# Kernel tuning notes

Measured on AMD Instinct MI355X. Metric: run time of the kernel, lower is better.

## Reference

```python
import jax, jax.numpy as jnp
import numpy as np

N_NODES = 50000
N_EDGES = 800000
F_NODE = 128
F_TASK = 128
HID = 64
HEADS = 4
BATCH = 16
NEG_SLOPE = 0.2


def setup_inputs() -> dict:
    key = jax.random.key(0)
    ks = jax.random.split(key, 20)
    rn = lambda k, sh, s=0.05: jax.random.normal(k, sh, dtype=jnp.float32) * s
    return {
        "x": rn(ks[0], (N_NODES, F_NODE), 1.0),
        "edge_index": jax.random.randint(ks[1], (2, N_EDGES), 0, N_NODES, dtype=jnp.int32),
        "task_feat": rn(ks[2], (BATCH, F_TASK), 1.0),
        # GAT layer 1 (F_NODE -> HEADS*HID, concat)
        "W1": rn(ks[3], (F_NODE, HEADS * HID)),
        "att_src1": rn(ks[4], (HEADS, HID)),
        "att_dst1": rn(ks[5], (HEADS, HID)),
        "b1": jnp.zeros((HEADS * HID,), jnp.float32),
        # GAT layer 2 (HEADS*HID -> HID, 1 head, mean/no-concat)
        "W2": rn(ks[6], (HEADS * HID, HID)),
        "att_src2": rn(ks[7], (1, HID)),
        "att_dst2": rn(ks[8], (1, HID)),
        "b2": jnp.zeros((HID,), jnp.float32),
        # task encoder MLP
        "te_W1": rn(ks[9], (F_TASK, HID)),
        "te_b1": jnp.zeros((HID,), jnp.float32),
        "te_W2": rn(ks[10], (HID, HID)),
        "te_b2": jnp.zeros((HID,), jnp.float32),
        # classifier MLP (2*HID -> HID -> 1)
        "cl_W1": rn(ks[11], (2 * HID, HID)),
        "cl_b1": jnp.zeros((HID,), jnp.float32),
        "cl_W2": rn(ks[12], (HID, 1)),
        "cl_b2": jnp.zeros((1,), jnp.float32),
    }


def _gat(x, src, dst, W, a_src, a_dst, bias, concat):
    """PyG-style GATConv: self-loops, per-dst segment softmax, scatter-add."""
    n = x.shape[0]
    heads, ch = a_src.shape
    h = (x @ W).reshape(n, heads, ch)                       # [N,H,C]
    alpha_s = jnp.einsum("nhc,hc->nh", h, a_src)            # [N,H]
    alpha_d = jnp.einsum("nhc,hc->nh", h, a_dst)
    loop = jnp.arange(n, dtype=src.dtype)                   # add self-loops
    s = jnp.concatenate([src, loop])
    d = jnp.concatenate([dst, loop])
    e = jax.nn.leaky_relu(alpha_s[s] + alpha_d[d], NEG_SLOPE)   # [E+N,H]
    m = jax.lax.stop_gradient(jax.ops.segment_max(e, d, num_segments=n))
    ex = jnp.exp(e - m[d])
    den = jax.ops.segment_sum(ex, d, num_segments=n)
    alpha = ex / (den[d] + 1e-16)                           # [E+N,H]
    out = jax.ops.segment_sum(h[s] * alpha[:, :, None], d, num_segments=n)
    out = out.reshape(n, heads * ch) if concat else out.mean(axis=1)
    return out + bias


def reference(x, edge_index, task_feat, W1, att_src1, att_dst1, b1,
              W2, att_src2, att_dst2, b2, te_W1, te_b1, te_W2, te_b2,
              cl_W1, cl_b1, cl_W2, cl_b2):
    src, dst = edge_index[0], edge_index[1]
    h = jax.nn.elu(_gat(x, src, dst, W1, att_src1, att_dst1, b1, True))
    h = jax.nn.elu(_gat(h, src, dst, W2, att_src2, att_dst2, b2, False))  # [N,HID]
    t = jax.nn.relu(task_feat @ te_W1 + te_b1) @ te_W2 + te_b2            # [B,HID]
    # classifier on concat([h_exp, t_exp]) == split first linear into two halves
    Wh, Wt = cl_W1[:HID], cl_W1[HID:]
    z = jax.nn.relu((h @ Wh)[None, :, :] + (t @ Wt)[:, None, :] + cl_b1)  # [B,N,HID]
    scores = (z @ cl_W2)[..., 0] + cl_b2[0]                               # [B,N]
    return scores
```

## Files before the change

### kernel.cpp

```cpp
#include <hip/hip_runtime.h>
#include <hip/hip_fp16.h>

#define NN 50000
#define NE 800000
#define FN 128
#define HH 256
#define HID 64
#define NBKT 196
#define CHUNK 4000
#define REGCAP 8192

typedef _Float16 f16x8 __attribute__((ext_vector_type(8)));
typedef float f32x4 __attribute__((ext_vector_type(4)));

__device__ __forceinline__ float lrelu(float v){ return v >= 0.f ? v : 0.2f * v; }
__device__ __forceinline__ float elu_(float v){ return v > 0.f ? v : expm1f(v); }

__device__ __forceinline__ void unp4(const float2 r, float& f0, float& f1, float& f2, float& f3){
  const __half2* hp = (const __half2*)&r;
  float2 a = __half22float2(hp[0]);
  float2 b = __half22float2(hp[1]);
  f0 = a.x; f1 = a.y; f2 = b.x; f3 = b.y;
}

__global__ void k_misc(const float* __restrict__ W2, const float* __restrict__ W1,
                       __half* __restrict__ Bp, __half* __restrict__ Bp1, __half* __restrict__ Bwh,
                       const float* __restrict__ task, const float* __restrict__ W1t,
                       const float* __restrict__ b1t, const float* __restrict__ W2t,
                       const float* __restrict__ b2t, const float* __restrict__ clW1,
                       const float* __restrict__ clb1, float* __restrict__ tWb,
                       int* __restrict__ binCnt){
  int bid = blockIdx.x, t = threadIdx.x;
  if (bid < 26){
    int f = bid * 256 + t;
    if (f < 2048){
      int lane = f & 63;
      int ct = (f >> 6) & 3, kt = f >> 8;
      int kbase = kt * 32 + (lane >> 4) * 8;
      int col = ct * 16 + (lane & 15);
#pragma unroll
      for (int i = 0; i < 8; ++i)
        Bp[(size_t)f * 8 + i] = (__half)W2[(kbase + i) * HID + col];
    } else if (f < 6144){
      int g = f - 2048;
      int lane = g & 63;
      int ct = (g >> 6) & 15, kt = g >> 10;
      int kbase = kt * 32 + (lane >> 4) * 8;
      int col = ct * 16 + (lane & 15);
#pragma unroll
      for (int i = 0; i < 8; ++i)
        Bp1[(size_t)g * 8 + i] = (__half)W1[(kbase + i) * HH + col];
    } else {
      int g = f - 6144;
      int lane = g & 63;
      int ct = (g >> 6) & 3, kt = g >> 8;
      int kbase = kt * 32 + (lane >> 4) * 8;
      int col = ct * 16 + (lane & 15);
#pragma unroll
      for (int i = 0; i < 8; ++i)
        Bwh[(size_t)g * 8 + i] = (__half)clW1[(kbase + i) * HID + col];
    }
  } else {
    binCnt[t] = 0;
    __shared__ float t1[16][64];
    __shared__ float t2[16][64];
    for (int idx = t; idx < 1024; idx += 256){
      int b = idx >> 6, c = idx & 63;
      float acc = b1t[c];
      for (int k = 0; k < 128; ++k) acc = fmaf(task[b*128 + k], W1t[k*64 + c], acc);
      t1[b][c] = fmaxf(acc, 0.f);
    }
    __syncthreads();
    for (int idx = t; idx < 1024; idx += 256){
      int b = idx >> 6, c = idx & 63;
      float acc = b2t[c];
      for (int k = 0; k < 64; ++k) acc = fmaf(t1[b][k], W2t[k*64 + c], acc);
      t2[b][c] = acc;
    }
    __syncthreads();
    for (int idx = t; idx < 1024; idx += 256){
      int b = idx >> 6, c = idx & 63;
      float acc = clb1[c];
      for (int k = 0; k < 64; ++k) acc = fmaf(t2[b][k], clW1[(64 + k)*64 + c], acc);
      tWb[idx] = acc;
    }
  }
}

__global__ void k_binGemm(const int* __restrict__ ei, int* __restrict__ binCnt,
                          unsigned* __restrict__ pr,
                          const float* __restrict__ x, const __half* __restrict__ Bp1,
                          const float* __restrict__ as1, const float* __restrict__ ad1,
                          __half* __restrict__ h1h, float* __restrict__ als, float* __restrict__ ald){
  __shared__ int hist[NBKT];
  __shared__ int lstart[NBKT];
  __shared__ int gpos[NBKT];
  __shared__ int cnt[NBKT];
  __shared__ unsigned stage[CHUNK];
  int bid = blockIdx.x, t = threadIdx.x;
  if (bid < 200){
    int e_base = bid * CHUNK;
    if (t < NBKT){ hist[t] = 0; cnt[t] = 0; }
    __syncthreads();
    for (int i = t; i < CHUNK; i += 256)
      atomicAdd(&hist[ei[NE + e_base + i] >> 8], 1);
    __syncthreads();
    {
      int lane = t & 63, wvi = t >> 6;
      int v = (t < NBKT) ? hist[t] : 0;
      int iv = v;
#pragma unroll
      for (int off = 1; off < 64; off <<= 1){
        int u = __shfl_up(iv, off);
        if (lane >= off) iv += u;
      }
      __shared__ int wsum[4];
      if (lane == 63) wsum[wvi] = iv;
      __syncthreads();
      int add = 0;
      for (int w = 0; w < wvi; ++w) add += wsum[w];
      iv += add;
      if (t < NBKT){
        lstart[t] = iv - v;
        gpos[t] = (v > 0) ? atomicAdd(&binCnt[t], v) : 0;
      }
    }
    __syncthreads();
    for (int i = t; i < CHUNK; i += 256){
      int e = e_base + i;
      int s = ei[e], d = ei[NE + e];
      int bb = d >> 8;
      int r = atomicAdd(&cnt[bb], 1);
      stage[lstart[bb] + r] = (unsigned)s | ((unsigned)(d & 255) << 16) | ((unsigned)bb << 24);
    }
    __syncthreads();
    for (int i = t; i < CHUNK; i += 256){
      unsigned p = stage[i];
      int bb = p >> 24;
      pr[(size_t)bb * REGCAP + gpos[bb] + (i - lstart[bb])] = p;
    }
    return;
  }
  int blk = bid - 200;
  int wv = t >> 6, lane = t & 63;
  int n0 = blk * 64 + wv * 16;
  int arow = n0 + (lane & 15);
  if (arow > NN - 1) arow = NN - 1;
  const float* xbase = x + (size_t)arow * FN + (lane >> 4) * 8;
  const f16x8* bbase = (const f16x8*)Bp1 + lane;

  f32x4 acc[16];
#pragma unroll
  for (int ct = 0; ct < 16; ++ct) acc[ct] = (f32x4){0.f,0.f,0.f,0.f};

#pragma unroll
  for (int kt = 0; kt < 4; ++kt){
    float4 xa = *(const float4*)(xbase + kt * 32);
    float4 xb = *(const float4*)(xbase + kt * 32 + 4);
    f16x8 a;
    a[0] = (_Float16)xa.x; a[1] = (_Float16)xa.y; a[2] = (_Float16)xa.z; a[3] = (_Float16)xa.w;
    a[4] = (_Float16)xb.x; a[5] = (_Float16)xb.y; a[6] = (_Float16)xb.z; a[7] = (_Float16)xb.w;
#pragma unroll
    for (int ct = 0; ct < 16; ++ct)
      acc[ct] = __builtin_amdgcn_mfma_f32_16x16x32_f16(a, bbase[(kt*16 + ct) * 64], acc[ct], 0, 0, 0);
  }

  int c4 = lane & 15, g4 = lane >> 4;
#pragma unroll
  for (int ct = 0; ct < 16; ++ct){
#pragma unroll
    for (int i = 0; i < 4; ++i){
      int n = n0 + g4 * 4 + i;
      if (n < NN) h1h[(size_t)n * HH + ct * 16 + c4] = (__half)acc[ct][i];
    }
  }
#pragma unroll
  for (int h = 0; h < 4; ++h){
    float sa0 = as1[(h*4+0)*16 + c4], sa1 = as1[(h*4+1)*16 + c4];
    float sa2 = as1[(h*4+2)*16 + c4], sa3 = as1[(h*4+3)*16 + c4];
    float da0 = ad1[(h*4+0)*16 + c4], da1 = ad1[(h*4+1)*16 + c4];
    float da2 = ad1[(h*4+2)*16 + c4], da3 = ad1[(h*4+3)*16 + c4];
#pragma unroll
    for (int i = 0; i < 4; ++i){
      float vs = acc[h*4+0][i]*sa0 + acc[h*4+1][i]*sa1 + acc[h*4+2][i]*sa2 + acc[h*4+3][i]*sa3;
      float vd = acc[h*4+0][i]*da0 + acc[h*4+1][i]*da1 + acc[h*4+2][i]*da2 + acc[h*4+3][i]*da3;
#pragma unroll
      for (int off = 1; off < 16; off <<= 1){
        vs += __shfl_xor(vs, off);
        vd += __shfl_xor(vd, off);
      }
      if (c4 == 0){
        int n = n0 + g4 * 4 + i;
        if (n < NN){ als[n*4 + h] = vs; ald[n*4 + h] = vd; }
      }
    }
  }
}

__global__ void k_rsplace(const int* __restrict__ binCnt, const unsigned* __restrict__ pr,
                          int* __restrict__ rs, int* __restrict__ csr){
  __shared__ int bbase[256];
  __shared__ int hist[256];
  __shared__ int lp[256];
  __shared__ int wsA[4];
  __shared__ int wsB[4];
  int b = blockIdx.x, t = threadIdx.x;
  int lane = t & 63, wv = t >> 6;
  {
    int v = (t < NBKT) ? binCnt[t] : 0;
    int iv = v;
#pragma unroll
    for (int off = 1; off < 64; off <<= 1){
      int u = __shfl_up(iv, off);
      if (lane >= off) iv += u;
    }
    if (lane == 63) wsA[wv] = iv;
    __syncthreads();
    int add = 0;
    for (int w = 0; w < wv; ++w) add += wsA[w];
    bbase[t] = iv + add - v;
    hist[t] = 0;
  }
  __syncthreads();
  int myBase = bbase[b];
  int myCnt  = binCnt[b];
  const unsigned* reg = pr + (size_t)b * REGCAP;
  for (int i = t; i < myCnt; i += 256)
    atomicAdd(&hist[(reg[i] >> 16) & 255], 1);
  __syncthreads();
  int excl;
  {
    int v = hist[t];
    int iv = v;
#pragma unroll
    for (int off = 1; off < 64; off <<= 1){
      int u = __shfl_up(iv, off);
      if (lane >= off) iv += u;
    }
    if (lane == 63) wsB[wv] = iv;
    __syncthreads();
    int add = 0;
    for (int w = 0; w < wv; ++w) add += wsB[w];
    excl = myBase + iv + add - v;
    lp[t] = excl;
  }
  int idx = b * 256 + t;
  if (idx < NN) rs[idx] = excl;
  if (b == 0 && t == 0) rs[NN] = NE;
  __syncthreads();
  for (int i = t; i < myCnt; i += 256){
    unsigned p = reg[i];
    int pos = atomicAdd(&lp[(p >> 16) & 255], 1);
    csr[pos] = (int)(p & 0xFFFFu);
  }
}

__global__ void k_agg1m(const int* __restrict__ rs, const int* __restrict__ csr,
                        const __half* __restrict__ h1h, const float* __restrict__ als,
                        const float* __restrict__ ald, const float* __restrict__ b1,
                        __half* __restrict__ g1h){
  int t = threadIdx.x, wv = t >> 6, lane = t & 63;
  int head = lane >> 4, q = lane & 15;
  int n = blockIdx.x * 4 + wv;
  int e0 = rs[n], e1 = rs[n + 1];
  int deg = e1 - e0;
  float adh = ald[n*4 + head];

  float w0r = 0.f, w1r = 0.f, w2r = 0.f, w3r = 0.f;
  int   s0r = 0,   s1r = 0,   s2r = 0,   s3r = 0;
  float den = 0.f;
  if (q      < deg){ s0r = csr[e0 + q];      w0r = expf(lrelu(als[s0r*4+head] + adh)); den += w0r; }
  if (q + 16 < deg){ s1r = csr[e0 + 16 + q]; w1r = expf(lrelu(als[s1r*4+head] + adh)); den += w1r; }
  if (q + 32 < deg){ s2r = csr[e0 + 32 + q]; w2r = expf(lrelu(als[s2r*4+head] + adh)); den += w2r; }
  if (q + 48 < deg){ s3r = csr[e0 + 48 + q]; w3r = expf(lrelu(als[s3r*4+head] + adh)); den += w3r; }
  for (int e = e0 + 64 + q; e < e1; e += 16) den += expf(lrelu(als[csr[e]*4+head] + adh));
  den += __shfl_xor(den, 1); den += __shfl_xor(den, 2);
  den += __shfl_xor(den, 4); den += __shfl_xor(den, 8);
  float selfw = expf(lrelu(als[n*4+head] + adh));
  float inv = 1.f / (den + selfw + 1e-16f);
  float wself = selfw * inv;

  float a0, a1, a2, a3;
  { float2 r = *(const float2*)(h1h + (size_t)n * HH + lane * 4);
    float f0,f1,f2,f3; unp4(r, f0,f1,f2,f3);
    a0 = wself*f0; a1 = wself*f1; a2 = wself*f2; a3 = wself*f3; }

  int hb = lane & 48;
  int cnt = deg < 64 ? deg : 64;
  auto pass = [&](float wp, int sp, int off){
    int lim = cnt - off; if (lim <= 0) return; if (lim > 16) lim = 16;
    for (int q2 = 0; q2 < lim; q2 += 4){
      int j1 = q2 + 1, j2 = q2 + 2, j3 = q2 + 3;
      float m1 = (j1 < lim) ? inv : 0.f; if (j1 >= lim) j1 = q2;
      float m2 = (j2 < lim) ? inv : 0.f; if (j2 >= lim) j2 = q2;
      float m3 = (j3 < lim) ? inv : 0.f; if (j3 >= lim) j3 = q2;
      float wa = inv * __shfl(wp, hb + q2); int sa = __shfl(sp, hb + q2);
      float wb = m1  * __shfl(wp, hb + j1); int sb = __shfl(sp, hb + j1);
      float wc = m2  * __shfl(wp, hb + j2); int sc = __shfl(sp, hb + j2);
      float wd = m3  * __shfl(wp, hb + j3); int sd = __shfl(sp, hb + j3);
      float2 ra = *(const float2*)(h1h + (size_t)sa * HH + lane * 4);
      float2 rb = *(const float2*)(h1h + (size_t)sb * HH + lane * 4);
      float2 rc = *(const float2*)(h1h + (size_t)sc * HH + lane * 4);
      float2 rd = *(const float2*)(h1h + (size_t)sd * HH + lane * 4);
      float f0,f1,f2,f3;
      unp4(ra, f0,f1,f2,f3); a0=fmaf(wa,f0,a0); a1=fmaf(wa,f1,a1); a2=fmaf(wa,f2,a2); a3=fmaf(wa,f3,a3);
      unp4(rb, f0,f1,f2,f3); a0=fmaf(wb,f0,a0); a1=fmaf(wb,f1,a1); a2=fmaf(wb,f2,a2); a3=fmaf(wb,f3,a3);
      unp4(rc, f0,f1,f2,f3); a0=fmaf(wc,f0,a0); a1=fmaf(wc,f1,a1); a2=fmaf(wc,f2,a2); a3=fmaf(wc,f3,a3);
      unp4(rd, f0,f1,f2,f3); a0=fmaf(wd,f0,a0); a1=fmaf(wd,f1,a1); a2=fmaf(wd,f2,a2); a3=fmaf(wd,f3,a3);
    }
  };
  pass(w0r, s0r, 0); pass(w1r, s1r, 16); pass(w2r, s2r, 32); pass(w3r, s3r, 48);
  for (int e = e0 + 64; e < e1; ++e){
    int s = csr[e];
    float w = inv * expf(lrelu(als[s*4+head] + adh));
    float2 r = *(const float2*)(h1h + (size_t)s * HH + lane * 4);
    float f0,f1,f2,f3; unp4(r, f0,f1,f2,f3);
    a0=fmaf(w,f0,a0); a1=fmaf(w,f1,a1); a2=fmaf(w,f2,a2); a3=fmaf(w,f3,a3);
  }

  float4 b4 = *(const float4*)(b1 + lane * 4);
  __half2 p0 = __floats2half2_rn(elu_(a0 + b4.x), elu_(a1 + b4.y));
  __half2 p1 = __floats2half2_rn(elu_(a2 + b4.z), elu_(a3 + b4.w));
  float2 outv; ((__half2*)&outv)[0] = p0; ((__half2*)&outv)[1] = p1;
  *(float2*)(g1h + (size_t)n * HH + lane * 4) = outv;
}

__global__ void k_gemm2m(const __half* __restrict__ g1h, const __half* __restrict__ Bp,
                         const float* __restrict__ as2, const float* __restrict__ ad2,
                         __half* __restrict__ h2h, float* __restrict__ als2, float* __restrict__ ald2){
  int t = threadIdx.x, wv = t >> 6, lane = t & 63;
  int n0 = blockIdx.x * 64 + wv * 16;
  int arow = n0 + (lane & 15);
  if (arow > NN - 1) arow = NN - 1;
  const _Float16* gbase = (const _Float16*)g1h + (size_t)arow * HH + (lane >> 4) * 8;
  const f16x8* bbase = (const f16x8*)Bp + lane;

  f32x4 acc0 = {0.f,0.f,0.f,0.f}, acc1 = {0.f,0.f,0.f,0.f};
  f32x4 acc2 = {0.f,0.f,0.f,0.f}, acc3 = {0.f,0.f,0.f,0.f};
#pragma unroll
  for (int kt = 0; kt < 8; ++kt){
    f16x8 a = *(const f16x8*)(gbase + kt * 32);
    acc0 = __builtin_amdgcn_mfma_f32_16x16x32_f16(a, bbase[(kt*4 + 0) * 64], acc0, 0, 0, 0);
    acc1 = __builtin_amdgcn_mfma_f32_16x16x32_f16(a, bbase[(kt*4 + 1) * 64], acc1, 0, 0, 0);
    acc2 = __builtin_amdgcn_mfma_f32_16x16x32_f16(a, bbase[(kt*4 + 2) * 64], acc2, 0, 0, 0);
    acc3 = __builtin_amdgcn_mfma_f32_16x16x32_f16(a, bbase[(kt*4 + 3) * 64], acc3, 0, 0, 0);
  }
  int c4 = lane & 15, g4 = lane >> 4;
  float as2v0 = as2[c4], as2v1 = as2[16 + c4], as2v2 = as2[32 + c4], as2v3 = as2[48 + c4];
  float ad2v0 = ad2[c4], ad2v1 = ad2[16 + c4], ad2v2 = ad2[32 + c4], ad2v3 = ad2[48 + c4];
  float vs[4], vd[4];
#pragma unroll
  for (int i = 0; i < 4; ++i){
    int n = n0 + g4 * 4 + i;
    if (n < NN){
      h2h[(size_t)n * HID + c4]      = (__half)acc0[i];
      h2h[(size_t)n * HID + 16 + c4] = (__half)acc1[i];
      h2h[(size_t)n * HID + 32 + c4] = (__half)acc2[i];
      h2h[(size_t)n * HID + 48 + c4] = (__half)acc3[i];
    }
    vs[i] = acc0[i]*as2v0 + acc1[i]*as2v1 + acc2[i]*as2v2 + acc3[i]*as2v3;
    vd[i] = acc0[i]*ad2v0 + acc1[i]*ad2v1 + acc2[i]*ad2v2 + acc3[i]*ad2v3;
  }
#pragma unroll
  for (int off = 1; off < 16; off <<= 1){
#pragma unroll
    for (int i = 0; i < 4; ++i){
      vs[i] += __shfl_xor(vs[i], off);
      vd[i] += __shfl_xor(vd[i], off);
    }
  }
  if (c4 == 0){
#pragma unroll
    for (int i = 0; i < 4; ++i){
      int n = n0 + g4 * 4 + i;
      if (n < NN){ als2[n] = vs[i]; ald2[n] = vd[i]; }
    }
  }
}

#define OSTRIDE 72
__global__ void k_agg2f(const int* __restrict__ rs, const int* __restrict__ csr,
                        const __half* __restrict__ h2h, const float* __restrict__ als,
                        const float* __restrict__ ald, const float* __restrict__ b2,
                        const __half* __restrict__ Bwh, const float* __restrict__ tWb,
                        const float* __restrict__ w2, const float* __restrict__ b2s,
                        float* __restrict__ out){
  __shared__ __half o_lds[64 * OSTRIDE];
  __shared__ float tws[1024];
  __shared__ float w2s[64];
  int t = threadIdx.x, lane = t & 63, wv = t >> 6;
  for (int i = t; i < 1024; i += 256) tws[i] = tWb[i];
  if (t < 64) w2s[t] = w2[t];

  int q = lane & 15;
  int g = t >> 4;
  int n0b = blockIdx.x * 64;
  int gb = lane & 48;
#pragma unroll 1
  for (int j = 0; j < 4; ++j){
    int nl = g * 4 + j;
    int n = n0b + nl;
    int nc = (n < NN) ? n : NN - 1;
    int e0 = rs[nc], e1 = rs[nc + 1];
    int deg = e1 - e0;
    float adn = ald[nc];

    float w0r = 0.f, w1r = 0.f, w2r = 0.f, w3r = 0.f;
    int   s0r = 0,   s1r = 0,   s2r = 0,   s3r = 0;
    float den = 0.f;
    if (q      < deg){ s0r = csr[e0 + q];      w0r = expf(lrelu(als[s0r] + adn)); den += w0r; }
    if (q + 16 < deg){ s1r = csr[e0 + 16 + q]; w1r = expf(lrelu(als[s1r] + adn)); den += w1r; }
    if (q + 32 < deg){ s2r = csr[e0 + 32 + q]; w2r = expf(lrelu(als[s2r] + adn)); den += w2r; }
    if (q + 48 < deg){ s3r = csr[e0 + 48 + q]; w3r = expf(lrelu(als[s3r] + adn)); den += w3r; }
    for (int e = e0 + 64 + q; e < e1; e += 16) den += expf(lrelu(als[csr[e]] + adn));
    den += __shfl_xor(den, 1); den += __shfl_xor(den, 2);
    den += __shfl_xor(den, 4); den += __shfl_xor(den, 8);
    float selfw = expf(lrelu(als[nc] + adn));
    float inv = 1.f / (den + selfw + 1e-16f);
    float wself = selfw * inv;

    float a0, a1, a2, a3;
    { float2 r = *(const float2*)(h2h + (size_t)nc * HID + q * 4);
      float f0,f1,f2,f3; unp4(r, f0,f1,f2,f3);
      a0 = wself*f0; a1 = wself*f1; a2 = wself*f2; a3 = wself*f3; }

    int dmax = deg;
    dmax = max(dmax, __shfl_xor(dmax, 16));
    dmax = max(dmax, __shfl_xor(dmax, 32));
    int cnt = dmax < 64 ? dmax : 64;
    auto pass = [&](float wp, int sp, int off){
      int lim = cnt - off; if (lim <= 0) return; if (lim > 16) lim = 16;
      for (int jj = 0; jj < lim; jj += 2){
        int j1 = (jj + 1 < lim) ? jj + 1 : jj;
        float mb = (jj + 1 < lim) ? inv : 0.f;
        float wa = inv * __shfl(wp, gb + jj); int sa = __shfl(sp, gb + jj);
        float wb = mb  * __shfl(wp, gb + j1); int sb = __shfl(sp, gb + j1);
        float2 ra = *(const float2*)(h2h + (size_t)sa * HID + q * 4);
        float2 rb = *(const float2*)(h2h + (size_t)sb * HID + q * 4);
        float f0,f1,f2,f3;
        unp4(ra, f0,f1,f2,f3); a0=fmaf(wa,f0,a0); a1=fmaf(wa,f1,a1); a2=fmaf(wa,f2,a2); a3=fmaf(wa,f3,a3);
        unp4(rb, f0,f1,f2,f3); a0=fmaf(wb,f0,a0); a1=fmaf(wb,f1,a1); a2=fmaf(wb,f2,a2); a3=fmaf(wb,f3,a3);
      }
    };
    pass(w0r, s0r, 0); pass(w1r, s1r, 16); pass(w2r, s2r, 32); pass(w3r, s3r, 48);
    for (int e = e0 + 64; e < e1; ++e){
      int s = csr[e];
      float w = inv * expf(lrelu(als[s] + adn));
      float2 r = *(const float2*)(h2h + (size_t)s * HID + q * 4);
      float f0,f1,f2,f3; unp4(r, f0,f1,f2,f3);
      a0=fmaf(w,f0,a0); a1=fmaf(w,f1,a1); a2=fmaf(w,f2,a2); a3=fmaf(w,f3,a3);
    }

    float4 b4 = *(const float4*)(b2 + q * 4);
    __half2 p0 = __floats2half2_rn(elu_(a0 + b4.x), elu_(a1 + b4.y));
    __half2 p1 = __floats2half2_rn(elu_(a2 + b4.z), elu_(a3 + b4.w));
    float2 outv; ((__half2*)&outv)[0] = p0; ((__half2*)&outv)[1] = p1;
    *(float2*)(o_lds + nl * OSTRIDE + q * 4) = outv;
  }
  __syncthreads();

  const _Float16* obase = (const _Float16*)o_lds + (wv * 16 + (lane & 15)) * OSTRIDE + (lane >> 4) * 8;
  const f16x8* bbase = (const f16x8*)Bwh + lane;

  f32x4 acc[4];
#pragma unroll
  for (int ct = 0; ct < 4; ++ct) acc[ct] = (f32x4){0.f,0.f,0.f,0.f};
#pragma unroll
  for (int kt = 0; kt < 2; ++kt){
    f16x8 a = *(const f16x8*)(obase + kt * 32);
#pragma unroll
    for (int ct = 0; ct < 4; ++ct)
      acc[ct] = __builtin_amdgcn_mfma_f32_16x16x32_f16(a, bbase[(kt*4 + ct) * 64], acc[ct], 0, 0, 0);
  }
  int c4 = lane & 15, g4 = lane >> 4;
  float wv0 = w2s[c4], wv1 = w2s[16 + c4], wv2 = w2s[32 + c4], wv3 = w2s[48 + c4];
  float bias = b2s[0];
#pragma unroll
  for (int i = 0; i < 4; ++i){
    int n = n0b + wv * 16 + g4 * 4 + i;
    float v[16];
#pragma unroll
    for (int b = 0; b < 16; ++b){
      const float* twb = tws + b * 64;
      v[b] = fmaxf(acc[0][i] + twb[c4], 0.f)      * wv0
           + fmaxf(acc[1][i] + twb[16 + c4], 0.f) * wv1
           + fmaxf(acc[2][i] + twb[32 + c4], 0.f) * wv2
           + fmaxf(acc[3][i] + twb[48 + c4], 0.f) * wv3;
    }
    bool h3 = (lane & 8) != 0;
    float u[8];
#pragma unroll
    for (int jj = 0; jj < 8; ++jj){
      float keep = h3 ? v[jj+8] : v[jj];
      float send = h3 ? v[jj]   : v[jj+8];
      u[jj] = keep + __shfl_xor(send, 8);
    }
    bool h2b = (lane & 4) != 0;
    float p[4];
#pragma unroll
    for (int jj = 0; jj < 4; ++jj){
      float keep = h2b ? u[jj+4] : u[jj];
      float send = h2b ? u[jj]   : u[jj+4];
      p[jj] = keep + __shfl_xor(send, 4);
    }
    bool h1b = (lane & 2) != 0;
    float qq[2];
#pragma unroll
    for (int jj = 0; jj < 2; ++jj){
      float keep = h1b ? p[jj+2] : p[jj];
      float send = h1b ? p[jj]   : p[jj+2];
      qq[jj] = keep + __shfl_xor(send, 2);
    }
    bool h0 = (lane & 1) != 0;
    float keep = h0 ? qq[1] : qq[0];
    float send = h0 ? qq[0] : qq[1];
    float z = keep + __shfl_xor(send, 1);
    if (n < NN) out[(size_t)c4 * NN + n] = z + bias;
  }
}

extern "C" void kernel_launch(void* const* d_in, const int* in_sizes, int n_in,
                              void* d_out, int out_size, void* d_ws, size_t ws_size,
                              hipStream_t stream){
  const float* x    = (const float*)d_in[0];
  const int*   ei   = (const int*)  d_in[1];
  const float* task = (const float*)d_in[2];
  const float* W1   = (const float*)d_in[3];
  const float* as1  = (const float*)d_in[4];
  const float* ad1  = (const float*)d_in[5];
  const float* b1   = (const float*)d_in[6];
  const float* W2   = (const float*)d_in[7];
  const float* as2  = (const float*)d_in[8];
  const float* ad2  = (const float*)d_in[9];
  const float* b2   = (const float*)d_in[10];
  const float* teW1 = (const float*)d_in[11];
  const float* teb1 = (const float*)d_in[12];
  const float* teW2 = (const float*)d_in[13];
  const float* teb2 = (const float*)d_in[14];
  const float* clW1 = (const float*)d_in[15];
  const float* clb1 = (const float*)d_in[16];
  const float* clW2 = (const float*)d_in[17];
  const float* clb2 = (const float*)d_in[18];
  float* out = (float*)d_out;
  float* ws  = (float*)d_ws;

  __half* h1h  = (__half*)ws;
  float* als1  = ws + 6400000;
  float* ald1  = als1 + 200000;
  __half* g1h  = (__half*)(ald1 + 200000);
  __half* h2h  = (__half*)(ald1 + 200000 + 6400000);
  float* als2  = ald1 + 200000 + 6400000 + 1600000;
  float* ald2  = als2 + 50000;
  float* tWb   = ald2 + 50000;
  int*   rs    = (int*)(tWb + 1024);
  int*   csr   = rs + 50004;
  int*   binCnt= csr + 800000;
  __half* Bp   = (__half*)(binCnt + 256);
  __half* Bp1  = Bp + 16384;
  __half* Bwh  = Bp1 + 32768;
  unsigned* pr = (unsigned*)(Bwh + 4096);

  k_misc   <<<27, 256, 0, stream>>>(W2, W1, Bp, Bp1, Bwh,
                                    task, teW1, teb1, teW2, teb2, clW1, clb1, tWb, binCnt);
  k_binGemm<<<200 + (NN + 63)/64, 256, 0, stream>>>(ei, binCnt, pr, x, Bp1,
                                                    as1, ad1, h1h, als1, ald1);
  k_rsplace<<<NBKT, 256, 0, stream>>>(binCnt, pr, rs, csr);
  k_agg1m  <<<12500, 256, 0, stream>>>(rs, csr, h1h, als1, ald1, b1, g1h);
  k_gemm2m <<<(NN + 63)/64, 256, 0, stream>>>(g1h, Bp, as2, ad2, h2h, als2, ald2);
  k_agg2f  <<<(NN + 63)/64, 256, 0, stream>>>(rs, csr, h2h, als2, ald2, b2,
                                              Bwh, tWb, clW2, clb2, out);
}
```

Baseline: 176.9 us.

## Split layer-1 aggregation into weight precompute and column-sliced gather kernels

The fused layer-1 attention aggregation is split in two. A first kernel computes the per-edge, per-head normalized softmax weights and writes them to a new workspace buffer. A second kernel does the weighted gather over 8 column slices of 32 features, with 8 lanes per node, so each block touches a narrower slice of h1 and may get better L2 reuse. The cost is an extra launch and about 12.8 MB of weight writes and re-reads, plus re-reading the CSR indices once per slice.

```diff
diff --git a/kernel.cpp b/kernel.cpp
--- a/kernel.cpp
+++ b/kernel.cpp
@@ -255,10 +255,9 @@
   }
 }
 
-__global__ void k_agg1m(const int* __restrict__ rs, const int* __restrict__ csr,
-                        const __half* __restrict__ h1h, const float* __restrict__ als,
-                        const float* __restrict__ ald, const float* __restrict__ b1,
-                        __half* __restrict__ g1h){
+__global__ void k_w1m(const int* __restrict__ rs, const int* __restrict__ csr,
+                      const float* __restrict__ als, const float* __restrict__ ald,
+                      float* __restrict__ w1p, float* __restrict__ wsp){
   int t = threadIdx.x, wv = t >> 6, lane = t & 63;
   int head = lane >> 4, q = lane & 15;
   int n = blockIdx.x * 4 + wv;
@@ -267,62 +266,69 @@
   float adh = ald[n*4 + head];
 
   float w0r = 0.f, w1r = 0.f, w2r = 0.f, w3r = 0.f;
-  int   s0r = 0,   s1r = 0,   s2r = 0,   s3r = 0;
   float den = 0.f;
-  if (q      < deg){ s0r = csr[e0 + q];      w0r = expf(lrelu(als[s0r*4+head] + adh)); den += w0r; }
-  if (q + 16 < deg){ s1r = csr[e0 + 16 + q]; w1r = expf(lrelu(als[s1r*4+head] + adh)); den += w1r; }
-  if (q + 32 < deg){ s2r = csr[e0 + 32 + q]; w2r = expf(lrelu(als[s2r*4+head] + adh)); den += w2r; }
-  if (q + 48 < deg){ s3r = csr[e0 + 48 + q]; w3r = expf(lrelu(als[s3r*4+head] + adh)); den += w3r; }
+  if (q      < deg){ w0r = expf(lrelu(als[csr[e0 + q]*4+head]      + adh)); den += w0r; }
+  if (q + 16 < deg){ w1r = expf(lrelu(als[csr[e0 + 16 + q]*4+head] + adh)); den += w1r; }
+  if (q + 32 < deg){ w2r = expf(lrelu(als[csr[e0 + 32 + q]*4+head] + adh)); den += w2r; }
+  if (q + 48 < deg){ w3r = expf(lrelu(als[csr[e0 + 48 + q]*4+head] + adh)); den += w3r; }
   for (int e = e0 + 64 + q; e < e1; e += 16) den += expf(lrelu(als[csr[e]*4+head] + adh));
   den += __shfl_xor(den, 1); den += __shfl_xor(den, 2);
   den += __shfl_xor(den, 4); den += __shfl_xor(den, 8);
   float selfw = expf(lrelu(als[n*4+head] + adh));
   float inv = 1.f / (den + selfw + 1e-16f);
-  float wself = selfw * inv;
+  float* wpl = w1p + (size_t)head * NE;
+  if (q == 0) wsp[head * NN + n] = selfw * inv;
+  if (q      < deg) wpl[e0 + q]      = w0r * inv;
+  if (q + 16 < deg) wpl[e0 + 16 + q] = w1r * inv;
+  if (q + 32 < deg) wpl[e0 + 32 + q] = w2r * inv;
+  if (q + 48 < deg) wpl[e0 + 48 + q] = w3r * inv;
+  for (int e = e0 + 64 + q; e < e1; e += 16)
+    wpl[e] = expf(lrelu(als[csr[e]*4+head] + adh)) * inv;
+}
+
+__global__ void k_agg1s(const int* __restrict__ rs, const int* __restrict__ csr,
+                        const __half* __restrict__ h1h, const float* __restrict__ w1p,
+                        const float* __restrict__ wsp, const float* __restrict__ b1,
+                        __half* __restrict__ g1h){
+  int t = threadIdx.x;
+  int slice = blockIdx.x & 7;
+  int head = slice >> 1;
+  int grp = t >> 3, ln8 = t & 7;
+  int n = (blockIdx.x >> 3) * 32 + grp;
+  if (n >= NN) return;
+  int co = slice * 32 + ln8 * 4;
 
   float a0, a1, a2, a3;
-  { float2 r = *(const float2*)(h1h + (size_t)n * HH + lane * 4);
+  { float wsf = wsp[head * NN + n];
+    float2 r = *(const float2*)(h1h + (size_t)n * HH + co);
     float f0,f1,f2,f3; unp4(r, f0,f1,f2,f3);
-    a0 = wself*f0; a1 = wself*f1; a2 = wself*f2; a3 = wself*f3; }
-
-  int hb = lane & 48;
-  int cnt = deg < 64 ? deg : 64;
-  auto pass = [&](float wp, int sp, int off){
-    int lim = cnt - off; if (lim <= 0) return; if (lim > 16) lim = 16;
-    for (int q2 = 0; q2 < lim; q2 += 4){
-      int j1 = q2 + 1, j2 = q2 + 2, j3 = q2 + 3;
-      float m1 = (j1 < lim) ? inv : 0.f; if (j1 >= lim) j1 = q2;
-      float m2 = (j2 < lim) ? inv : 0.f; if (j2 >= lim) j2 = q2;
-      float m3 = (j3 < lim) ? inv : 0.f; if (j3 >= lim) j3 = q2;
-      float wa = inv * __shfl(wp, hb + q2); int sa = __shfl(sp, hb + q2);
-      float wb = m1  * __shfl(wp, hb + j1); int sb = __shfl(sp, hb + j1);
-      float wc = m2  * __shfl(wp, hb + j2); int sc = __shfl(sp, hb + j2);
-      float wd = m3  * __shfl(wp, hb + j3); int sd = __shfl(sp, hb + j3);
-      float2 ra = *(const float2*)(h1h + (size_t)sa * HH + lane * 4);
-      float2 rb = *(const float2*)(h1h + (size_t)sb * HH + lane * 4);
-      float2 rc = *(const float2*)(h1h + (size_t)sc * HH + lane * 4);
-      float2 rd = *(const float2*)(h1h + (size_t)sd * HH + lane * 4);
-      float f0,f1,f2,f3;
-      unp4(ra, f0,f1,f2,f3); a0=fmaf(wa,f0,a0); a1=fmaf(wa,f1,a1); a2=fmaf(wa,f2,a2); a3=fmaf(wa,f3,a3);
-      unp4(rb, f0,f1,f2,f3); a0=fmaf(wb,f0,a0); a1=fmaf(wb,f1,a1); a2=fmaf(wb,f2,a2); a3=fmaf(wb,f3,a3);
-      unp4(rc, f0,f1,f2,f3); a0=fmaf(wc,f0,a0); a1=fmaf(wc,f1,a1); a2=fmaf(wc,f2,a2); a3=fmaf(wc,f3,a3);
-      unp4(rd, f0,f1,f2,f3); a0=fmaf(wd,f0,a0); a1=fmaf(wd,f1,a1); a2=fmaf(wd,f2,a2); a3=fmaf(wd,f3,a3);
-    }
-  };
-  pass(w0r, s0r, 0); pass(w1r, s1r, 16); pass(w2r, s2r, 32); pass(w3r, s3r, 48);
-  for (int e = e0 + 64; e < e1; ++e){
+    a0 = wsf*f0; a1 = wsf*f1; a2 = wsf*f2; a3 = wsf*f3; }
+
+  int e0 = rs[n], e1 = rs[n + 1];
+  const float* wpl = w1p + (size_t)head * NE;
+  int e = e0;
+  for (; e + 1 < e1; e += 2){
+    int s0 = csr[e], s1 = csr[e + 1];
+    float wa = wpl[e], wb = wpl[e + 1];
+    float2 r0 = *(const float2*)(h1h + (size_t)s0 * HH + co);
+    float2 r1 = *(const float2*)(h1h + (size_t)s1 * HH + co);
+    float f0,f1,f2,f3;
+    unp4(r0, f0,f1,f2,f3); a0=fmaf(wa,f0,a0); a1=fmaf(wa,f1,a1); a2=fmaf(wa,f2,a2); a3=fmaf(wa,f3,a3);
+    unp4(r1, f0,f1,f2,f3); a0=fmaf(wb,f0,a0); a1=fmaf(wb,f1,a1); a2=fmaf(wb,f2,a2); a3=fmaf(wb,f3,a3);
+  }
+  if (e < e1){
     int s = csr[e];
-    float w = inv * expf(lrelu(als[s*4+head] + adh));
-    float2 r = *(const float2*)(h1h + (size_t)s * HH + lane * 4);
+    float w = wpl[e];
+    float2 r = *(const float2*)(h1h + (size_t)s * HH + co);
     float f0,f1,f2,f3; unp4(r, f0,f1,f2,f3);
     a0=fmaf(w,f0,a0); a1=fmaf(w,f1,a1); a2=fmaf(w,f2,a2); a3=fmaf(w,f3,a3);
   }
 
-  float4 b4 = *(const float4*)(b1 + lane * 4);
+  float4 b4 = *(const float4*)(b1 + co);
   __half2 p0 = __floats2half2_rn(elu_(a0 + b4.x), elu_(a1 + b4.y));
   __half2 p1 = __floats2half2_rn(elu_(a2 + b4.z), elu_(a3 + b4.w));
   float2 outv; ((__half2*)&outv)[0] = p0; ((__half2*)&outv)[1] = p1;
-  *(float2*)(g1h + (size_t)n * HH + lane * 4) = outv;
+  *(float2*)(g1h + (size_t)n * HH + co) = outv;
 }
 
 __global__ void k_gemm2m(const __half* __restrict__ g1h, const __half* __restrict__ Bp,
@@ -559,13 +565,16 @@
   __half* Bp1  = Bp + 16384;
   __half* Bwh  = Bp1 + 32768;
   unsigned* pr = (unsigned*)(Bwh + 4096);
+  float* w1p   = (float*)(pr + NBKT * REGCAP);
+  float* wsp   = w1p + 4 * NE;
 
   k_misc   <<<27, 256, 0, stream>>>(W2, W1, Bp, Bp1, Bwh,
                                     task, teW1, teb1, teW2, teb2, clW1, clb1, tWb, binCnt);
   k_binGemm<<<200 + (NN + 63)/64, 256, 0, stream>>>(ei, binCnt, pr, x, Bp1,
                                                     as1, ad1, h1h, als1, ald1);
   k_rsplace<<<NBKT, 256, 0, stream>>>(binCnt, pr, rs, csr);
-  k_agg1m  <<<12500, 256, 0, stream>>>(rs, csr, h1h, als1, ald1, b1, g1h);
+  k_w1m    <<<12500, 256, 0, stream>>>(rs, csr, als1, ald1, w1p, wsp);
+  k_agg1s  <<<8 * ((NN + 31) / 32), 256, 0, stream>>>(rs, csr, h1h, w1p, wsp, b1, g1h);
   k_gemm2m <<<(NN + 63)/64, 256, 0, stream>>>(g1h, Bp, as2, ad2, h2h, als2, ald2);
   k_agg2f  <<<(NN + 63)/64, 256, 0, stream>>>(rs, csr, h2h, als2, ald2, b2,
                                               Bwh, tWb, clW2, clb2, out);
```

New measurement: 222.7 us. +25.9%, slower.
